# Performance work log

Hardware: AMD Instinct MI355X
Metric: run time of the kernel (lower is better)

## Reference

```python
import jax, jax.numpy as jnp
import numpy as np

D = 2048
H = 16
DH = D // H  # 128
B = 512
EPS = 1e-5


def _layernorm(x, g, b):
    m = jnp.mean(x, axis=-1, keepdims=True)
    v = jnp.mean((x - m) ** 2, axis=-1, keepdims=True)
    return (x - m) * jax.lax.rsqrt(v + EPS) * g + b


def setup_inputs() -> dict:
    key = jax.random.key(0)
    ks = jax.random.split(key, 16)
    s_in = 1.0 / np.sqrt(D)
    s_ff = 1.0 / np.sqrt(4 * D)
    return {
        "x": jax.random.normal(ks[0], (B, D), jnp.float32),
        # per-head q/k/v projections, stacked over heads: [H, D, DH]
        "Wq": jax.random.uniform(ks[1], (H, D, DH), jnp.float32, -s_in, s_in),
        "bq": jax.random.uniform(ks[2], (H, DH), jnp.float32, -s_in, s_in),
        "Wk": jax.random.uniform(ks[3], (H, D, DH), jnp.float32, -s_in, s_in),
        "bk": jax.random.uniform(ks[4], (H, DH), jnp.float32, -s_in, s_in),
        "Wv": jax.random.uniform(ks[5], (H, D, DH), jnp.float32, -s_in, s_in),
        "bv": jax.random.uniform(ks[6], (H, DH), jnp.float32, -s_in, s_in),
        "Wo": jax.random.uniform(ks[7], (D, D), jnp.float32, -s_in, s_in),
        "bo": jax.random.uniform(ks[8], (D,), jnp.float32, -s_in, s_in),
        "W1": jax.random.uniform(ks[9], (D, 4 * D), jnp.float32, -s_in, s_in),
        "b1": jax.random.uniform(ks[10], (4 * D,), jnp.float32, -s_in, s_in),
        "W2": jax.random.uniform(ks[11], (4 * D, D), jnp.float32, -s_ff, s_ff),
        "b2": jax.random.uniform(ks[12], (D,), jnp.float32, -s_ff, s_ff),
        "g1": jnp.ones((D,), jnp.float32),
        "be1": jnp.zeros((D,), jnp.float32),
        "g2": jnp.ones((D,), jnp.float32),
        "be2": jnp.zeros((D,), jnp.float32),
    }


def reference(x, Wq, bq, Wk, bk, Wv, bv, Wo, bo, W1, b1, W2, b2, g1, be1, g2, be2):
    # --- pre-norm attention branch ---
    h = _layernorm(x, g1, be1)                       # [B, D]
    q = jnp.einsum('bd,hde->bhe', h, Wq) + bq        # [B, H, DH]
    k = jnp.einsum('bd,hde->bhe', h, Wk) + bk
    v = jnp.einsum('bd,hde->bhe', h, Wv) + bv
    # outer-product 'attention' per sample: [B, H, DH, DH]
    attn = q[..., :, None] * k[..., None, :] / jnp.sqrt(jnp.float32(DH))
    attn = jax.nn.softmax(attn, axis=-1)
    o = jnp.einsum('bhij,bhj->bhi', attn, v)         # [B, H, DH]
    o = o.reshape(x.shape[0], H * DH)                # concat over heads
    x = x + o @ Wo + bo
    # --- pre-norm FFN branch ---
    h2 = _layernorm(x, g2, be2)
    x = x + jax.nn.relu(h2 @ W1 + b1) @ W2 + b2
    return x
```

## Files before the change

kernel.cpp:

```cpp
#include <hip/hip_runtime.h>
#include <hip/hip_bf16.h>
#include <math.h>


#define DDIM 2048
#define HHEADS 16
#define DHEAD 128
#define BROWS 512
#define LN_EPS 1e-5f

typedef __bf16 bf16x8_t __attribute__((ext_vector_type(8)));
typedef float f32x4_t __attribute__((ext_vector_type(4)));

#define GLD16(gptr, lptr)                                                     \
    __builtin_amdgcn_global_load_lds(                                         \
        (const __attribute__((address_space(1))) void*)(gptr),                \
        (__attribute__((address_space(3))) void*)(lptr), 16, 0, 0)

__global__ __launch_bounds__(256) void ln_kernel(const float* __restrict__ x,
                                                 const float* __restrict__ g,
                                                 const float* __restrict__ b,
                                                 __bf16* __restrict__ out) {
    const int row = blockIdx.x;
    const int tid = threadIdx.x;
    const float4* x4 = (const float4*)(x + (size_t)row * DDIM);
    float4 a = x4[2 * tid];
    float4 c = x4[2 * tid + 1];
    float s  = a.x + a.y + a.z + a.w + c.x + c.y + c.z + c.w;
    float s2 = a.x*a.x + a.y*a.y + a.z*a.z + a.w*a.w
             + c.x*c.x + c.y*c.y + c.z*c.z + c.w*c.w;
    #pragma unroll
    for (int off = 32; off > 0; off >>= 1) {
        s  += __shfl_down(s, off);
        s2 += __shfl_down(s2, off);
    }
    __shared__ float ps[4], ps2[4];
    __shared__ float mean_s, rstd_s;
    const int lane = tid & 63, w = tid >> 6;
    if (lane == 0) { ps[w] = s; ps2[w] = s2; }
    __syncthreads();
    if (tid == 0) {
        float S  = ps[0] + ps[1] + ps[2] + ps[3];
        float S2 = ps2[0] + ps2[1] + ps2[2] + ps2[3];
        float m  = S * (1.0f / DDIM);
        float var = S2 * (1.0f / DDIM) - m * m;
        mean_s = m;
        rstd_s = rsqrtf(var + LN_EPS);
    }
    __syncthreads();
    const float m = mean_s, r = rstd_s;
    const float4* g4 = (const float4*)g;
    const float4* b4 = (const float4*)b;
    float4 ga = g4[2 * tid], gb = g4[2 * tid + 1];
    float4 ba = b4[2 * tid], bb = b4[2 * tid + 1];
    bf16x8_t o;
    o[0] = (__bf16)((a.x - m) * r * ga.x + ba.x);
    o[1] = (__bf16)((a.y - m) * r * ga.y + ba.y);
    o[2] = (__bf16)((a.z - m) * r * ga.z + ba.z);
    o[3] = (__bf16)((a.w - m) * r * ga.w + ba.w);
    o[4] = (__bf16)((c.x - m) * r * gb.x + bb.x);
    o[5] = (__bf16)((c.y - m) * r * gb.y + bb.y);
    o[6] = (__bf16)((c.z - m) * r * gb.z + bb.z);
    o[7] = (__bf16)((c.w - m) * r * gb.w + bb.w);
    *(bf16x8_t*)(out + (size_t)row * DDIM + tid * 8) = o;
}

__global__ __launch_bounds__(256) void transpose_kernel(
    const float* __restrict__ src, __bf16* __restrict__ dst, int R, int C) {
    __shared__ float tile[64][65];
    const size_t bofs = (size_t)blockIdx.z * R * C;
    src += bofs;
    dst += bofs;
    const int c0 = blockIdx.x * 64, r0 = blockIdx.y * 64;
    const int t = threadIdx.x;
    const int rr = t >> 4, cc = (t & 15) * 4;
    #pragma unroll
    for (int p = 0; p < 4; p++) {
        const float4 v =
            *(const float4*)(src + (size_t)(r0 + rr + 16 * p) * C + c0 + cc);
        tile[rr + 16 * p][cc]     = v.x;
        tile[rr + 16 * p][cc + 1] = v.y;
        tile[rr + 16 * p][cc + 2] = v.z;
        tile[rr + 16 * p][cc + 3] = v.w;
    }
    __syncthreads();
    const int slot = t & 7;
    #pragma unroll
    for (int p = 0; p < 2; p++) {
        const int c = (t >> 3) + 32 * p;
        bf16x8_t o;
        #pragma unroll
        for (int j = 0; j < 8; j++)
            o[j] = (__bf16)tile[slot * 8 + j][c];
        *(bf16x8_t*)(dst + (size_t)(c0 + c) * R + r0 + slot * 8) = o;
    }
}

__global__ __launch_bounds__(256) void transpose_qkv_kernel(
    const float* __restrict__ Wq, const float* __restrict__ Wk,
    const float* __restrict__ Wv, __bf16* __restrict__ dstall) {
    __shared__ float tile[64][65];
    const int z = blockIdx.z, which = z >> 4, hd = z & 15;
    const float* src = (which == 0) ? Wq : (which == 1) ? Wk : Wv;
    src += (size_t)hd * DDIM * DHEAD;
    __bf16* dst = dstall + (size_t)which * DDIM * DDIM + (size_t)hd * DDIM * DHEAD;
    const int R = DDIM, C = DHEAD;
    const int c0 = blockIdx.x * 64, r0 = blockIdx.y * 64;
    const int t = threadIdx.x;
    const int rr = t >> 4, cc = (t & 15) * 4;
    #pragma unroll
    for (int p = 0; p < 4; p++) {
        const float4 v =
            *(const float4*)(src + (size_t)(r0 + rr + 16 * p) * C + c0 + cc);
        tile[rr + 16 * p][cc]     = v.x;
        tile[rr + 16 * p][cc + 1] = v.y;
        tile[rr + 16 * p][cc + 2] = v.z;
        tile[rr + 16 * p][cc + 3] = v.w;
    }
    __syncthreads();
    const int slot = t & 7;
    #pragma unroll
    for (int p = 0; p < 2; p++) {
        const int c = (t >> 3) + 32 * p;
        bf16x8_t o;
        #pragma unroll
        for (int j = 0; j < 8; j++)
            o[j] = (__bf16)tile[slot * 8 + j][c];
        *(bf16x8_t*)(dst + (size_t)(c0 + c) * R + r0 + slot * 8) = o;
    }
}

template <int SPLITZ, int OUT_BF16, int RELU, int RES, int BIAS3>
__global__ __launch_bounds__(512) void gemm_bt(
    const __bf16* __restrict__ A, int K,
    const __bf16* __restrict__ Bt,
    const float* __restrict__ bias, const float* __restrict__ biasB,
    const float* __restrict__ biasC,
    const float* __restrict__ Res,
    void* __restrict__ Cout, int N) {
    constexpr int TM = 128, TN = 128, DEPTH = 4;
    constexpr int STG = (TM + TN) * 64;
    __shared__ __align__(16) __bf16 smem[DEPTH * STG];

    const int tid = threadIdx.x;
    const int w = tid >> 6, lane = tid & 63;

    const int gx = gridDim.x, gy = gridDim.y, gz = gridDim.z;
    {
    }
    int l = blockIdx.x + gx * (blockIdx.y + gy * blockIdx.z);
    const int xcd = l & 7;
    int i0 = l >> 3;
    const int by = i0 % gy; i0 /= gy;
    const int bz = i0 % gz; i0 /= gz;
    const int bx = xcd * (gx >> 3) + i0;

    const int m0 = by * TM, n0 = bx * TN;

    const int Kloc = K / SPLITZ;
    const int kb = bz * Kloc;
    const int NK = Kloc / 64;

    constexpr int NT = (TM + TN) / 8;
    constexpr int NI = NT / 8;

    const int srow = lane >> 3;
    const int sslot = (lane & 7) ^ srow;

    const __bf16* srcs[NI];
    int toff[NI];
    #pragma unroll
    for (int i = 0; i < NI; i++) {
        const int t = w + 8 * i;
        toff[i] = t * 512;
        const int r = t * 8 + srow;
        srcs[i] = (r < TM)
                      ? A + (size_t)(m0 + r) * K + kb + sslot * 8
                      : Bt + (size_t)(n0 + r - TM) * K + kb + sslot * 8;
    }

    constexpr int MI = 4, NJ = 4;
    const int wg = w & 3, kh = w >> 2;
    const int wm = (wg >> 1) * 64, wn = (wg & 1) * 64;
    const int fm = lane & 15, quad = lane >> 4;
    const int f7 = fm & 7;

    const int sl = ((kh * 4 + quad) ^ f7) * 16;
    int aoff[MI], boff[NJ];
    #pragma unroll
    for (int i = 0; i < MI; i++)
        aoff[i] = (wm + 16 * i + fm) * 128 + sl;
    #pragma unroll
    for (int j = 0; j < NJ; j++)
        boff[j] = (TM + wn + 16 * j + fm) * 128 + sl;

    f32x4_t acc[MI][NJ] = {};

    #pragma unroll
    for (int d = 0; d < DEPTH; d++)
        #pragma unroll
        for (int i = 0; i < NI; i++)
            GLD16(srcs[i] + d * 64, smem + d * STG + toff[i]);

    for (int ks = 0; ks < NK; ks++) {
        const char* st = (const char*)smem + (ks % DEPTH) * (STG * 2);
        if (ks < NK - 2)
            asm volatile("s_waitcnt vmcnt(%0)\n\ts_barrier"
                         :: "i"((DEPTH - 2) * NI) : "memory");
        else if (ks == NK - 2)
            asm volatile("s_waitcnt vmcnt(%0)\n\ts_barrier"
                         :: "i"(NI) : "memory");
        else
            asm volatile("s_waitcnt vmcnt(0)\n\ts_barrier" ::: "memory");

        if (ks >= 1 && ks + DEPTH - 1 < NK) {
            __bf16* dst = smem + ((ks - 1) % DEPTH) * STG;
            #pragma unroll
            for (int i = 0; i < NI; i++)
                GLD16(srcs[i] + (size_t)(ks + DEPTH - 1) * 64, dst + toff[i]);
        }

        bf16x8_t a[MI], b[NJ];
        #pragma unroll
        for (int i = 0; i < MI; i++)
            a[i] = *(const bf16x8_t*)(st + aoff[i]);
        #pragma unroll
        for (int j = 0; j < NJ; j++)
            b[j] = *(const bf16x8_t*)(st + boff[j]);
        __builtin_amdgcn_s_setprio(1);
        #pragma unroll
        for (int i = 0; i < MI; i++)
            #pragma unroll
            for (int j = 0; j < NJ; j++)
                acc[i][j] = __builtin_amdgcn_mfma_f32_16x16x32_bf16(
                    a[i], b[j], acc[i][j], 0, 0, 0);
        __builtin_amdgcn_s_setprio(0);
    }

    char* mrg = (char*)smem + wg * 16384;
    __syncthreads();
    if (kh == 1) {
        #pragma unroll
        for (int i = 0; i < MI; i++)
            #pragma unroll
            for (int j = 0; j < NJ; j++)
                *(f32x4_t*)(mrg + (((i * NJ + j) * 64) + lane) * 16) = acc[i][j];
    }
    __syncthreads();
    if (kh == 1) return;
    #pragma unroll
    for (int i = 0; i < MI; i++)
        #pragma unroll
        for (int j = 0; j < NJ; j++) {
            const f32x4_t p = *(const f32x4_t*)(mrg + (((i * NJ + j) * 64) + lane) * 16);
            acc[i][j][0] += p[0]; acc[i][j][1] += p[1];
            acc[i][j][2] += p[2]; acc[i][j][3] += p[3];
        }

    if (SPLITZ > 1) {
        float* P = (float*)Cout + (size_t)bz * (gy * TM) * N;
        #pragma unroll
        for (int i = 0; i < MI; i++)
            #pragma unroll
            for (int j = 0; j < NJ; j++) {
                const int col = n0 + wn + 16 * j + fm;
                #pragma unroll
                for (int r = 0; r < 4; r++) {
                    const int row = m0 + wm + 16 * i + quad * 4 + r;
                    P[(size_t)row * N + col] = acc[i][j][r];
                }
            }
    } else {
        const float* bp = bias;
        if (BIAS3) {
            const int seg = n0 >> 11;
            bp = (seg == 0) ? bias : (seg == 1) ? biasB : biasC;
        }
        #pragma unroll
        for (int i = 0; i < MI; i++)
            #pragma unroll
            for (int j = 0; j < NJ; j++) {
                const int col = n0 + wn + 16 * j + fm;
                const float bcol = BIAS3 ? bp[col & 2047] : bp[col];
                #pragma unroll
                for (int r = 0; r < 4; r++) {
                    const int row = m0 + wm + 16 * i + quad * 4 + r;
                    float val = acc[i][j][r] + bcol;
                    if (RES) val += Res[(size_t)row * N + col];
                    if (RELU) val = fmaxf(val, 0.0f);
                    if (OUT_BF16)
                        ((__bf16*)Cout)[(size_t)row * N + col] = (__bf16)val;
                    else
                        ((float*)Cout)[(size_t)row * N + col] = val;
                }
            }
    }
}

template <int NS>
__global__ __launch_bounds__(256) void reduce_splitk(
    const float* __restrict__ part, const float* __restrict__ Res,
    const float* __restrict__ bias, float* __restrict__ out) {
    const int idx = blockIdx.x * 256 + threadIdx.x;
    const float4 b4 = ((const float4*)bias)[idx & 511];
    float4 r = ((const float4*)Res)[idx];
    #pragma unroll
    for (int s = 0; s < NS; s++) {
        const float4 p = ((const float4*)part)[(size_t)s * 262144 + idx];
        r.x += p.x; r.y += p.y; r.z += p.z; r.w += p.w;
    }
    r.x += b4.x; r.y += b4.y; r.z += b4.z; r.w += b4.w;
    ((float4*)out)[idx] = r;
}

template <int NS>
__global__ __launch_bounds__(256) void reduce_ln_kernel(
    const float* __restrict__ part, const float* __restrict__ x,
    const float* __restrict__ bo, const float* __restrict__ g,
    const float* __restrict__ be, float* __restrict__ x1,
    __bf16* __restrict__ h2) {
    const int row = blockIdx.x;
    const int tid = threadIdx.x;
    const size_t rbase = (size_t)row * DDIM;
    float v[8];
    #pragma unroll
    for (int p = 0; p < 2; p++) {
        const int c = tid * 8 + p * 4;
        float4 r = *(const float4*)(x + rbase + c);
        const float4 b4 = *(const float4*)(bo + c);
        r.x += b4.x; r.y += b4.y; r.z += b4.z; r.w += b4.w;
        #pragma unroll
        for (int s = 0; s < NS; s++) {
            const float4 q = *(const float4*)(part + (size_t)s * BROWS * DDIM + rbase + c);
            r.x += q.x; r.y += q.y; r.z += q.z; r.w += q.w;
        }
        *(float4*)(x1 + rbase + c) = r;
        v[p * 4 + 0] = r.x; v[p * 4 + 1] = r.y; v[p * 4 + 2] = r.z; v[p * 4 + 3] = r.w;
    }
    float s = 0.f, s2 = 0.f;
    #pragma unroll
    for (int i = 0; i < 8; i++) { s += v[i]; s2 += v[i] * v[i]; }
    #pragma unroll
    for (int off = 32; off > 0; off >>= 1) {
        s  += __shfl_down(s, off);
        s2 += __shfl_down(s2, off);
    }
    __shared__ float ps[4], ps2[4];
    __shared__ float mean_s, rstd_s;
    const int lane = tid & 63, wv = tid >> 6;
    if (lane == 0) { ps[wv] = s; ps2[wv] = s2; }
    __syncthreads();
    if (tid == 0) {
        float S  = ps[0] + ps[1] + ps[2] + ps[3];
        float S2 = ps2[0] + ps2[1] + ps2[2] + ps2[3];
        float m  = S * (1.0f / DDIM);
        float var = S2 * (1.0f / DDIM) - m * m;
        mean_s = m;
        rstd_s = rsqrtf(var + LN_EPS);
    }
    __syncthreads();
    const float m = mean_s, r = rstd_s;
    const float4* g4 = (const float4*)g;
    const float4* b4 = (const float4*)be;
    float4 ga = g4[2 * tid], gb = g4[2 * tid + 1];
    float4 ba = b4[2 * tid], bb = b4[2 * tid + 1];
    bf16x8_t o;
    o[0] = (__bf16)((v[0] - m) * r * ga.x + ba.x);
    o[1] = (__bf16)((v[1] - m) * r * ga.y + ba.y);
    o[2] = (__bf16)((v[2] - m) * r * ga.z + ba.z);
    o[3] = (__bf16)((v[3] - m) * r * ga.w + ba.w);
    o[4] = (__bf16)((v[4] - m) * r * gb.x + bb.x);
    o[5] = (__bf16)((v[5] - m) * r * gb.y + bb.y);
    o[6] = (__bf16)((v[6] - m) * r * gb.z + bb.z);
    o[7] = (__bf16)((v[7] - m) * r * gb.w + bb.w);
    *(bf16x8_t*)(h2 + rbase + tid * 8) = o;
}

__global__ __launch_bounds__(128) void attn_kernel(
    const __bf16* __restrict__ qkv, __bf16* __restrict__ o) {
    const int bh = blockIdx.x;
    const int b = bh >> 4, h = bh & 15;
    const size_t base = (size_t)b * (3 * DDIM) + h * DHEAD;
    const int tid = threadIdx.x;
    __shared__ float ks[DHEAD], vs[DHEAD];
    ks[tid] = (float)qkv[base + DDIM + tid];
    vs[tid] = (float)qkv[base + 2 * DDIM + tid];
    __syncthreads();
    const float a = (float)qkv[base + tid] * 0.08838834764831845f;
    float den = 0.0f, num = 0.0f;
    #pragma unroll 8
    for (int j = 0; j < DHEAD; j++) {
        float e = __expf(a * ks[j]);
        den += e;
        num += e * vs[j];
    }
    o[(size_t)b * DDIM + h * DHEAD + tid] = (__bf16)(num / den);
}

extern "C" void kernel_launch(void* const* d_in, const int* in_sizes, int n_in,
                              void* d_out, int out_size, void* d_ws, size_t ws_size,
                              hipStream_t stream) {
    const float* x   = (const float*)d_in[0];
    const float* Wq  = (const float*)d_in[1];
    const float* bq  = (const float*)d_in[2];
    const float* Wk  = (const float*)d_in[3];
    const float* bk  = (const float*)d_in[4];
    const float* Wv  = (const float*)d_in[5];
    const float* bv  = (const float*)d_in[6];
    const float* Wo  = (const float*)d_in[7];
    const float* bo  = (const float*)d_in[8];
    const float* W1  = (const float*)d_in[9];
    const float* b1  = (const float*)d_in[10];
    const float* W2  = (const float*)d_in[11];
    const float* b2  = (const float*)d_in[12];
    const float* g1  = (const float*)d_in[13];
    const float* be1 = (const float*)d_in[14];
    const float* g2  = (const float*)d_in[15];
    const float* be2 = (const float*)d_in[16];
    float* out = (float*)d_out;

    char* base = (char*)d_ws;
    __bf16* bt_qkv = (__bf16*)(base + 32768);
    char*   slotA  = base + 32768 + 25165824;
    char*   slotB  = slotA + 33554432;
    __bf16* h   = (__bf16*)(slotB + 0);
    __bf16* qkv = (__bf16*)(slotB + 2097152);
    __bf16* ob  = (__bf16*)(slotB + 8388608);
    float*  woP = (float*)(slotB + 10485760);
    float*  w2P = (float*)(slotB + 0);
    float*  x1  = (float*)((char*)bt_qkv + 0);
    __bf16* h2  = (__bf16*)((char*)bt_qkv + 4194304);
    __bf16* t   = (__bf16*)((char*)bt_qkv + 6291456);
    __bf16* Wot = (__bf16*)slotA;
    __bf16* W1t = (__bf16*)slotB;
    __bf16* W2t = (__bf16*)slotA;

    transpose_qkv_kernel<<<dim3(2, 32, 48), 256, 0, stream>>>(Wq, Wk, Wv, bt_qkv);
    transpose_kernel<<<dim3(32, 32, 1), 256, 0, stream>>>(Wo, Wot, DDIM, DDIM);

    ln_kernel<<<BROWS, 256, 0, stream>>>(x, g1, be1, h);

    gemm_bt<1, 1, 0, 0, 1><<<dim3(48, 4), 512, 0, stream>>>(
        h, DDIM, bt_qkv, bq, bk, bv, nullptr, qkv, 3 * DDIM);

    attn_kernel<<<BROWS * HHEADS, 128, 0, stream>>>(qkv, ob);

    gemm_bt<4, 0, 0, 0, 0><<<dim3(16, 4, 4), 512, 0, stream>>>(
        ob, DDIM, Wot, nullptr, nullptr, nullptr, nullptr, woP, DDIM);
    reduce_ln_kernel<4><<<BROWS, 256, 0, stream>>>(woP, x, bo, g2, be2, x1, h2);

    transpose_kernel<<<dim3(128, 32, 1), 256, 0, stream>>>(W1, W1t, DDIM, 4 * DDIM);
    transpose_kernel<<<dim3(32, 128, 1), 256, 0, stream>>>(W2, W2t, 4 * DDIM, DDIM);

    gemm_bt<1, 1, 1, 0, 0><<<dim3(64, 4), 512, 0, stream>>>(
        h2, DDIM, W1t, b1, nullptr, nullptr, nullptr, t, 4 * DDIM);

    gemm_bt<4, 0, 0, 0, 0><<<dim3(16, 4, 4), 512, 0, stream>>>(
        t, 4 * DDIM, W2t, nullptr, nullptr, nullptr, nullptr, w2P, DDIM);
    reduce_splitk<4><<<1024, 256, 0, stream>>>(w2P, x1, b2, out);
}
```

Measured before the change: 351.6 us.

## Fuse all weight transposes and first layernorm into one prep kernel; retile Wo GEMM

All six weight transpose/convert launches and the first layernorm are merged into a single prep_kernel launch dispatched by block index, and the workspace is relaid out so every transposed weight has its own buffer. The gemm_bt template now takes tile sizes, and the Wo projection uses 64x64 tiles without split-K, writing x + o@Wo + bo directly through the RES epilogue. That removes the partial-sum buffer and the reduce_ln kernel, which is replaced by a plain ln_kernel on x1. This cuts launch count and partial-buffer traffic. In exchange the Wo GEMM uses smaller tiles over the full K, and the workspace grows.

Measured after the change: 353.4 us. No clear change (+0.5%).

```diff
diff --git a/kernel.cpp b/kernel.cpp
--- a/kernel.cpp
+++ b/kernel.cpp
@@ -65,72 +65,109 @@
     *(bf16x8_t*)(out + (size_t)row * DDIM + tid * 8) = o;
 }
 
-__global__ __launch_bounds__(256) void transpose_kernel(
-    const float* __restrict__ src, __bf16* __restrict__ dst, int R, int C) {
-    __shared__ float tile[64][65];
-    const size_t bofs = (size_t)blockIdx.z * R * C;
-    src += bofs;
-    dst += bofs;
-    const int c0 = blockIdx.x * 64, r0 = blockIdx.y * 64;
+__global__ __launch_bounds__(256) void prep_kernel(
+    const float* __restrict__ Wq, const float* __restrict__ Wk,
+    const float* __restrict__ Wv, const float* __restrict__ Wo,
+    const float* __restrict__ W1, const float* __restrict__ W2,
+    const float* __restrict__ x, const float* __restrict__ g1,
+    const float* __restrict__ be1,
+    __bf16* __restrict__ bt_qkv, __bf16* __restrict__ Wot,
+    __bf16* __restrict__ W1t, __bf16* __restrict__ W2t,
+    __bf16* __restrict__ h) {
+    __shared__ __align__(16) float tile[64 * 65];
+    const int bid = blockIdx.x;
     const int t = threadIdx.x;
-    const int rr = t >> 4, cc = (t & 15) * 4;
-    #pragma unroll
-    for (int p = 0; p < 4; p++) {
-        const float4 v =
-            *(const float4*)(src + (size_t)(r0 + rr + 16 * p) * C + c0 + cc);
-        tile[rr + 16 * p][cc]     = v.x;
-        tile[rr + 16 * p][cc + 1] = v.y;
-        tile[rr + 16 * p][cc + 2] = v.z;
-        tile[rr + 16 * p][cc + 3] = v.w;
-    }
-    __syncthreads();
-    const int slot = t & 7;
-    #pragma unroll
-    for (int p = 0; p < 2; p++) {
-        const int c = (t >> 3) + 32 * p;
+    if (bid < 12288) {
+        const float* src;
+        __bf16* dst;
+        int R, C, r0, c0;
+        if (bid < 3072) {
+            const int z = bid >> 6, rem = bid & 63;
+            const int which = z >> 4, hd = z & 15;
+            src = ((which == 0) ? Wq : (which == 1) ? Wk : Wv) +
+                  (size_t)hd * DDIM * DHEAD;
+            dst = bt_qkv + (size_t)which * DDIM * DDIM +
+                  (size_t)hd * DDIM * DHEAD;
+            R = DDIM; C = DHEAD;
+            c0 = (rem & 1) * 64; r0 = (rem >> 1) * 64;
+        } else if (bid < 4096) {
+            const int local = bid - 3072;
+            src = Wo; dst = Wot; R = DDIM; C = DDIM;
+            c0 = (local & 31) * 64; r0 = (local >> 5) * 64;
+        } else if (bid < 8192) {
+            const int local = bid - 4096;
+            src = W1; dst = W1t; R = DDIM; C = 4 * DDIM;
+            c0 = (local & 127) * 64; r0 = (local >> 7) * 64;
+        } else {
+            const int local = bid - 8192;
+            src = W2; dst = W2t; R = 4 * DDIM; C = DDIM;
+            c0 = (local & 31) * 64; r0 = (local >> 5) * 64;
+        }
+        const int rr = t >> 4, cc = (t & 15) * 4;
+        #pragma unroll
+        for (int p = 0; p < 4; p++) {
+            const float4 v =
+                *(const float4*)(src + (size_t)(r0 + rr + 16 * p) * C + c0 + cc);
+            tile[(rr + 16 * p) * 65 + cc]     = v.x;
+            tile[(rr + 16 * p) * 65 + cc + 1] = v.y;
+            tile[(rr + 16 * p) * 65 + cc + 2] = v.z;
+            tile[(rr + 16 * p) * 65 + cc + 3] = v.w;
+        }
+        __syncthreads();
+        const int slot = t & 7;
+        #pragma unroll
+        for (int p = 0; p < 2; p++) {
+            const int c = (t >> 3) + 32 * p;
+            bf16x8_t o;
+            #pragma unroll
+            for (int j = 0; j < 8; j++)
+                o[j] = (__bf16)tile[(slot * 8 + j) * 65 + c];
+            *(bf16x8_t*)(dst + (size_t)(c0 + c) * R + r0 + slot * 8) = o;
+        }
+    } else {
+        const int row = bid - 12288;
+        const float4* x4 = (const float4*)(x + (size_t)row * DDIM);
+        float4 a = x4[2 * t];
+        float4 c = x4[2 * t + 1];
+        float s  = a.x + a.y + a.z + a.w + c.x + c.y + c.z + c.w;
+        float s2 = a.x*a.x + a.y*a.y + a.z*a.z + a.w*a.w
+                 + c.x*c.x + c.y*c.y + c.z*c.z + c.w*c.w;
+        #pragma unroll
+        for (int off = 32; off > 0; off >>= 1) {
+            s  += __shfl_down(s, off);
+            s2 += __shfl_down(s2, off);
+        }
+        const int lane = t & 63, w = t >> 6;
+        if (lane == 0) { tile[w] = s; tile[8 + w] = s2; }
+        __syncthreads();
+        if (t == 0) {
+            float S  = tile[0] + tile[1] + tile[2] + tile[3];
+            float S2 = tile[8] + tile[9] + tile[10] + tile[11];
+            float m  = S * (1.0f / DDIM);
+            float var = S2 * (1.0f / DDIM) - m * m;
+            tile[16] = m;
+            tile[17] = rsqrtf(var + LN_EPS);
+        }
+        __syncthreads();
+        const float m = tile[16], r = tile[17];
+        const float4* g4 = (const float4*)g1;
+        const float4* b4 = (const float4*)be1;
+        float4 ga = g4[2 * t], gb = g4[2 * t + 1];
+        float4 ba = b4[2 * t], bb = b4[2 * t + 1];
         bf16x8_t o;
-        #pragma unroll
-        for (int j = 0; j < 8; j++)
-            o[j] = (__bf16)tile[slot * 8 + j][c];
-        *(bf16x8_t*)(dst + (size_t)(c0 + c) * R + r0 + slot * 8) = o;
-    }
-}
-
-__global__ __launch_bounds__(256) void transpose_qkv_kernel(
-    const float* __restrict__ Wq, const float* __restrict__ Wk,
-    const float* __restrict__ Wv, __bf16* __restrict__ dstall) {
-    __shared__ float tile[64][65];
-    const int z = blockIdx.z, which = z >> 4, hd = z & 15;
-    const float* src = (which == 0) ? Wq : (which == 1) ? Wk : Wv;
-    src += (size_t)hd * DDIM * DHEAD;
-    __bf16* dst = dstall + (size_t)which * DDIM * DDIM + (size_t)hd * DDIM * DHEAD;
-    const int R = DDIM, C = DHEAD;
-    const int c0 = blockIdx.x * 64, r0 = blockIdx.y * 64;
-    const int t = threadIdx.x;
-    const int rr = t >> 4, cc = (t & 15) * 4;
-    #pragma unroll
-    for (int p = 0; p < 4; p++) {
-        const float4 v =
-            *(const float4*)(src + (size_t)(r0 + rr + 16 * p) * C + c0 + cc);
-        tile[rr + 16 * p][cc]     = v.x;
-        tile[rr + 16 * p][cc + 1] = v.y;
-        tile[rr + 16 * p][cc + 2] = v.z;
-        tile[rr + 16 * p][cc + 3] = v.w;
-    }
-    __syncthreads();
-    const int slot = t & 7;
-    #pragma unroll
-    for (int p = 0; p < 2; p++) {
-        const int c = (t >> 3) + 32 * p;
-        bf16x8_t o;
-        #pragma unroll
-        for (int j = 0; j < 8; j++)
-            o[j] = (__bf16)tile[slot * 8 + j][c];
-        *(bf16x8_t*)(dst + (size_t)(c0 + c) * R + r0 + slot * 8) = o;
-    }
-}
-
-template <int SPLITZ, int OUT_BF16, int RELU, int RES, int BIAS3>
+        o[0] = (__bf16)((a.x - m) * r * ga.x + ba.x);
+        o[1] = (__bf16)((a.y - m) * r * ga.y + ba.y);
+        o[2] = (__bf16)((a.z - m) * r * ga.z + ba.z);
+        o[3] = (__bf16)((a.w - m) * r * ga.w + ba.w);
+        o[4] = (__bf16)((c.x - m) * r * gb.x + bb.x);
+        o[5] = (__bf16)((c.y - m) * r * gb.y + bb.y);
+        o[6] = (__bf16)((c.z - m) * r * gb.z + bb.z);
+        o[7] = (__bf16)((c.w - m) * r * gb.w + bb.w);
+        *(bf16x8_t*)(h + (size_t)row * DDIM + t * 8) = o;
+    }
+}
+
+template <int TM, int TN, int SPLITZ, int OUT_BF16, int RELU, int RES, int BIAS3>
 __global__ __launch_bounds__(512) void gemm_bt(
     const __bf16* __restrict__ A, int K,
     const __bf16* __restrict__ Bt,
@@ -138,7 +175,7 @@
     const float* __restrict__ biasC,
     const float* __restrict__ Res,
     void* __restrict__ Cout, int N) {
-    constexpr int TM = 128, TN = 128, DEPTH = 4;
+    constexpr int DEPTH = 4;
     constexpr int STG = (TM + TN) * 64;
     __shared__ __align__(16) __bf16 smem[DEPTH * STG];
 
@@ -146,8 +183,6 @@
     const int w = tid >> 6, lane = tid & 63;
 
     const int gx = gridDim.x, gy = gridDim.y, gz = gridDim.z;
-    {
-    }
     int l = blockIdx.x + gx * (blockIdx.y + gy * blockIdx.z);
     const int xcd = l & 7;
     int i0 = l >> 3;
@@ -171,17 +206,17 @@
     int toff[NI];
     #pragma unroll
     for (int i = 0; i < NI; i++) {
-        const int t = w + 8 * i;
-        toff[i] = t * 512;
-        const int r = t * 8 + srow;
+        const int tt = w + 8 * i;
+        toff[i] = tt * 512;
+        const int r = tt * 8 + srow;
         srcs[i] = (r < TM)
                       ? A + (size_t)(m0 + r) * K + kb + sslot * 8
                       : Bt + (size_t)(n0 + r - TM) * K + kb + sslot * 8;
     }
 
-    constexpr int MI = 4, NJ = 4;
+    constexpr int MI = TM / 32, NJ = TN / 32;
     const int wg = w & 3, kh = w >> 2;
-    const int wm = (wg >> 1) * 64, wn = (wg & 1) * 64;
+    const int wm = (wg >> 1) * (TM / 2), wn = (wg & 1) * (TN / 2);
     const int fm = lane & 15, quad = lane >> 4;
     const int f7 = fm & 7;
 
@@ -237,7 +272,7 @@
         __builtin_amdgcn_s_setprio(0);
     }
 
-    char* mrg = (char*)smem + wg * 16384;
+    char* mrg = (char*)smem + wg * (MI * NJ * 64 * 16);
     __syncthreads();
     if (kh == 1) {
         #pragma unroll
@@ -311,69 +346,6 @@
     }
     r.x += b4.x; r.y += b4.y; r.z += b4.z; r.w += b4.w;
     ((float4*)out)[idx] = r;
-}
-
-template <int NS>
-__global__ __launch_bounds__(256) void reduce_ln_kernel(
-    const float* __restrict__ part, const float* __restrict__ x,
-    const float* __restrict__ bo, const float* __restrict__ g,
-    const float* __restrict__ be, float* __restrict__ x1,
-    __bf16* __restrict__ h2) {
-    const int row = blockIdx.x;
-    const int tid = threadIdx.x;
-    const size_t rbase = (size_t)row * DDIM;
-    float v[8];
-    #pragma unroll
-    for (int p = 0; p < 2; p++) {
-        const int c = tid * 8 + p * 4;
-        float4 r = *(const float4*)(x + rbase + c);
-        const float4 b4 = *(const float4*)(bo + c);
-        r.x += b4.x; r.y += b4.y; r.z += b4.z; r.w += b4.w;
-        #pragma unroll
-        for (int s = 0; s < NS; s++) {
-            const float4 q = *(const float4*)(part + (size_t)s * BROWS * DDIM + rbase + c);
-            r.x += q.x; r.y += q.y; r.z += q.z; r.w += q.w;
-        }
-        *(float4*)(x1 + rbase + c) = r;
-        v[p * 4 + 0] = r.x; v[p * 4 + 1] = r.y; v[p * 4 + 2] = r.z; v[p * 4 + 3] = r.w;
-    }
-    float s = 0.f, s2 = 0.f;
-    #pragma unroll
-    for (int i = 0; i < 8; i++) { s += v[i]; s2 += v[i] * v[i]; }
-    #pragma unroll
-    for (int off = 32; off > 0; off >>= 1) {
-        s  += __shfl_down(s, off);
-        s2 += __shfl_down(s2, off);
-    }
-    __shared__ float ps[4], ps2[4];
-    __shared__ float mean_s, rstd_s;
-    const int lane = tid & 63, wv = tid >> 6;
-    if (lane == 0) { ps[wv] = s; ps2[wv] = s2; }
-    __syncthreads();
-    if (tid == 0) {
-        float S  = ps[0] + ps[1] + ps[2] + ps[3];
-        float S2 = ps2[0] + ps2[1] + ps2[2] + ps2[3];
-        float m  = S * (1.0f / DDIM);
-        float var = S2 * (1.0f / DDIM) - m * m;
-        mean_s = m;
-        rstd_s = rsqrtf(var + LN_EPS);
-    }
-    __syncthreads();
-    const float m = mean_s, r = rstd_s;
-    const float4* g4 = (const float4*)g;
-    const float4* b4 = (const float4*)be;
-    float4 ga = g4[2 * tid], gb = g4[2 * tid + 1];
-    float4 ba = b4[2 * tid], bb = b4[2 * tid + 1];
-    bf16x8_t o;
-    o[0] = (__bf16)((v[0] - m) * r * ga.x + ba.x);
-    o[1] = (__bf16)((v[1] - m) * r * ga.y + ba.y);
-    o[2] = (__bf16)((v[2] - m) * r * ga.z + ba.z);
-    o[3] = (__bf16)((v[3] - m) * r * ga.w + ba.w);
-    o[4] = (__bf16)((v[4] - m) * r * gb.x + bb.x);
-    o[5] = (__bf16)((v[5] - m) * r * gb.y + bb.y);
-    o[6] = (__bf16)((v[6] - m) * r * gb.z + bb.z);
-    o[7] = (__bf16)((v[7] - m) * r * gb.w + bb.w);
-    *(bf16x8_t*)(h2 + rbase + tid * 8) = o;
 }
 
 __global__ __launch_bounds__(128) void attn_kernel(
@@ -420,42 +392,36 @@
     float* out = (float*)d_out;
 
     char* base = (char*)d_ws;
-    __bf16* bt_qkv = (__bf16*)(base + 32768);
-    char*   slotA  = base + 32768 + 25165824;
-    char*   slotB  = slotA + 33554432;
-    __bf16* h   = (__bf16*)(slotB + 0);
-    __bf16* qkv = (__bf16*)(slotB + 2097152);
-    __bf16* ob  = (__bf16*)(slotB + 8388608);
-    float*  woP = (float*)(slotB + 10485760);
-    float*  w2P = (float*)(slotB + 0);
-    float*  x1  = (float*)((char*)bt_qkv + 0);
-    __bf16* h2  = (__bf16*)((char*)bt_qkv + 4194304);
-    __bf16* t   = (__bf16*)((char*)bt_qkv + 6291456);
-    __bf16* Wot = (__bf16*)slotA;
-    __bf16* W1t = (__bf16*)slotB;
-    __bf16* W2t = (__bf16*)slotA;
-
-    transpose_qkv_kernel<<<dim3(2, 32, 48), 256, 0, stream>>>(Wq, Wk, Wv, bt_qkv);
-    transpose_kernel<<<dim3(32, 32, 1), 256, 0, stream>>>(Wo, Wot, DDIM, DDIM);
-
-    ln_kernel<<<BROWS, 256, 0, stream>>>(x, g1, be1, h);
-
-    gemm_bt<1, 1, 0, 0, 1><<<dim3(48, 4), 512, 0, stream>>>(
+    __bf16* bt_qkv = (__bf16*)(base + 0);
+    __bf16* Wot    = (__bf16*)(base + 25165824);
+    __bf16* W1t    = (__bf16*)(base + 33554432);
+    __bf16* W2t    = (__bf16*)(base + 67108864);
+    __bf16* h      = (__bf16*)(base + 100663296);
+    __bf16* qkv    = (__bf16*)(base + 102760448);
+    __bf16* ob     = (__bf16*)(base + 109051904);
+    float*  x1     = (float*)(base + 111149056);
+    __bf16* h2     = (__bf16*)(base + 115343360);
+    __bf16* t      = (__bf16*)(base + 117440512);
+    float*  w2P    = (float*)(base + 125829120);
+
+    prep_kernel<<<12800, 256, 0, stream>>>(Wq, Wk, Wv, Wo, W1, W2, x, g1, be1,
+                                           bt_qkv, Wot, W1t, W2t, h);
+
+    gemm_bt<128, 128, 1, 1, 0, 0, 1><<<dim3(48, 4), 512, 0, stream>>>(
         h, DDIM, bt_qkv, bq, bk, bv, nullptr, qkv, 3 * DDIM);
 
     attn_kernel<<<BROWS * HHEADS, 128, 0, stream>>>(qkv, ob);
 
-    gemm_bt<4, 0, 0, 0, 0><<<dim3(16, 4, 4), 512, 0, stream>>>(
-        ob, DDIM, Wot, nullptr, nullptr, nullptr, nullptr, woP, DDIM);
-    reduce_ln_kernel<4><<<BROWS, 256, 0, stream>>>(woP, x, bo, g2, be2, x1, h2);
-
-    transpose_kernel<<<dim3(128, 32, 1), 256, 0, stream>>>(W1, W1t, DDIM, 4 * DDIM);
-    transpose_kernel<<<dim3(32, 128, 1), 256, 0, stream>>>(W2, W2t, 4 * DDIM, DDIM);
-
-    gemm_bt<1, 1, 1, 0, 0><<<dim3(64, 4), 512, 0, stream>>>(
+    gemm_bt<64, 64, 1, 0, 0, 1, 0><<<dim3(32, 8), 512, 0, stream>>>(
+        ob, DDIM, Wot, bo, nullptr, nullptr, x, x1, DDIM);
+
+    ln_kernel<<<BROWS, 256, 0, stream>>>(x1, g2, be2, h2);
+
+    gemm_bt<128, 128, 1, 1, 1, 0, 0><<<dim3(64, 4), 512, 0, stream>>>(
         h2, DDIM, W1t, b1, nullptr, nullptr, nullptr, t, 4 * DDIM);
 
-    gemm_bt<4, 0, 0, 0, 0><<<dim3(16, 4, 4), 512, 0, stream>>>(
+    gemm_bt<128, 128, 4, 0, 0, 0, 0><<<dim3(16, 4, 4), 512, 0, stream>>>(
         t, 4 * DDIM, W2t, nullptr, nullptr, nullptr, nullptr, w2P, DDIM);
+
     reduce_splitk<4><<<1024, 256, 0, stream>>>(w2P, x1, b2, out);
 }
```
